# Kernel tuning notes

Hardware: AMD Instinct MI355X
Metric: run time of the kernel (lower is better)

## Reference

```python
import jax, jax.numpy as jnp
import numpy as np

D_STATE = 128   # Mamba2 default (the SS2D d_state=16 is never forwarded to Mamba2)
N_HEADS = 4     # d_ssm // headdim = d_model / (d_model//4)
D_CONV = 4
EPS = 1e-5


def silu(v):
    return v * jax.nn.sigmoid(v)


def setup_inputs() -> dict:
    key = jax.random.key(0)
    ks = jax.random.split(key, 12)
    d_model = 256
    d_inner = 2 * d_model            # expand=2
    d_ssm = d_model
    conv_dim = d_ssm + 2 * D_STATE   # 512
    d_in_proj = 2 * d_inner + 2 * D_STATE + N_HEADS  # 1284
    B, H, W = 8, 64, 64
    inp = {
        "x": jax.random.normal(ks[0], (B, d_model, H, W), jnp.float32),
        "in_proj_w": jax.random.normal(ks[1], (d_in_proj, d_model), jnp.float32) * 0.02,
        "conv_w": jax.random.normal(ks[2], (conv_dim, D_CONV), jnp.float32) * 0.2,
        "conv_b": jnp.zeros((conv_dim,), jnp.float32),
        "dt_bias": jax.random.normal(ks[3], (N_HEADS,), jnp.float32) * 0.1,
        "A_log": jnp.log(jax.random.uniform(ks[4], (N_HEADS,), jnp.float32, 1.0, 16.0)),
        "D": jax.random.normal(ks[5], (N_HEADS,), jnp.float32),
        "norm_w": jnp.ones((d_ssm,), jnp.float32),
        "out_proj_w": jax.random.normal(ks[6], (d_model, d_inner), jnp.float32) * 0.02,
        "se_w1": jax.random.normal(ks[7], (d_model // 4, d_model), jnp.float32) * 0.05,
        "se_b1": jnp.zeros((d_model // 4,), jnp.float32),
        "se_w2": jax.random.normal(ks[8], (d_model, d_model // 4), jnp.float32) * 0.05,
        "se_b2": jnp.zeros((d_model,), jnp.float32),
    }
    return inp


def _forward(x, in_proj_w, conv_w, conv_b, dt_bias, A_log, D, norm_w,
             out_proj_w, se_w1, se_b1, se_w2, se_b2):
    Bb, C, H, W = x.shape
    L = H * W
    d_model = C
    d_inner = 2 * d_model
    d_ssm = d_model
    d_mlp = d_inner - d_ssm
    headdim = d_ssm // N_HEADS
    conv_dim = d_ssm + 2 * D_STATE

    u = x.reshape(Bb, C, L).transpose(0, 2, 1)              # (b, l, c)
    zxbcdt = u @ in_proj_w.T                                 # (b, l, 1284)
    z0 = zxbcdt[..., :d_mlp]
    x0 = zxbcdt[..., d_mlp:2 * d_mlp]
    z = zxbcdt[..., 2 * d_mlp:2 * d_mlp + d_ssm]
    xBC = zxbcdt[..., 2 * d_mlp + d_ssm:2 * d_mlp + d_ssm + conv_dim]
    dt = zxbcdt[..., -N_HEADS:]

    dt = jax.nn.softplus(dt + dt_bias)                       # (b, l, h)

    # causal depthwise conv along l, kernel size D_CONV
    xpad = jnp.pad(xBC, ((0, 0), (D_CONV - 1, 0), (0, 0)))
    xconv = conv_b
    for k in range(D_CONV):
        xconv = xconv + xpad[:, k:k + L, :] * conv_w[:, k]
    xconv = silu(xconv)

    xs = xconv[..., :d_ssm]
    Bm = xconv[..., d_ssm:d_ssm + D_STATE]                   # (b, l, n) ngroups=1
    Cm = xconv[..., d_ssm + D_STATE:]                        # (b, l, n)
    xh = xs.reshape(Bb, L, N_HEADS, headdim)                 # (b, l, h, p)

    A = -jnp.exp(A_log)                                      # (h,)

    def step(hstate, inp):
        xt, dtt, Bt, Ct = inp  # (b,h,p), (b,h), (b,n), (b,n)
        dA = jnp.exp(dtt * A)                                # (b, h)
        hstate = hstate * dA[:, :, None, None] + \
            (dtt[:, :, None, None] * xt[..., None]) * Bt[:, None, None, :]
        y = jnp.einsum('bhpn,bn->bhp', hstate, Ct)
        return hstate, y

    h0 = jnp.zeros((Bb, N_HEADS, headdim, D_STATE), x.dtype)
    _, ys = jax.lax.scan(
        step, h0,
        (xh.transpose(1, 0, 2, 3), dt.transpose(1, 0, 2),
         Bm.transpose(1, 0, 2), Cm.transpose(1, 0, 2)))
    y = ys.transpose(1, 0, 2, 3)                             # (b, l, h, p)
    y = y + D[None, None, :, None] * xh                      # skip
    y = y.reshape(Bb, L, d_ssm)

    # gated RMSNorm (norm_before_gate=False): gate then normalize
    y = y * silu(z)
    y = y * jax.lax.rsqrt(jnp.mean(y * y, axis=-1, keepdims=True) + EPS) * norm_w

    y = jnp.concatenate([silu(z0) * x0, y], axis=-1)         # (b, l, d_inner)
    out = y @ out_proj_w.T                                   # (b, l, d_model)
    out = out.transpose(0, 2, 1).reshape(Bb, C, H, W)

    # SE-style spectral attention
    s = out.mean(axis=(2, 3))                                # (b, c)
    s = jax.nn.relu(s @ se_w1.T + se_b1)
    s = jax.nn.sigmoid(s @ se_w2.T + se_b2)
    return out * s[:, :, None, None]


def reference(x, in_proj_w, conv_w, conv_b, dt_bias, A_log, D, norm_w,
              out_proj_w, se_w1, se_b1, se_w2, se_b2):
    return _forward(x, in_proj_w, conv_w, conv_b, dt_bias, A_log, D, norm_w,
                    out_proj_w, se_w1, se_b1, se_w2, se_b2)
```

## Files before the change

### kernel.cpp

```cpp
#include <hip/hip_runtime.h>
#include <stdint.h>

typedef __attribute__((ext_vector_type(8))) short bf16x8;
typedef __attribute__((ext_vector_type(4))) float f32x4;

__device__ __forceinline__ float bf2f(unsigned short u) {
  unsigned int x = ((unsigned int)u) << 16;
  return __builtin_bit_cast(float, x);
}
__device__ __forceinline__ unsigned short f2bf(float f) {
  unsigned int x = __builtin_bit_cast(unsigned int, f);
  unsigned int r = x + 0x7FFFu + ((x >> 16) & 1u);
  return (unsigned short)(r >> 16);
}
__device__ __forceinline__ float silu(float v) { return v / (1.f + __expf(-v)); }
__device__ __forceinline__ f32x4 fz4() { f32x4 z; z[0]=0.f; z[1]=0.f; z[2]=0.f; z[3]=0.f; return z; }

#define LSEQ 4096
#define DMODEL 256
#define NIN 1284
#define NINP 1408

__global__ __launch_bounds__(256) void k_prep(const float* __restrict__ w_in,
                                              const float* __restrict__ w_out,
                                              unsigned short* __restrict__ wpad,
                                              unsigned short* __restrict__ woutbf,
                                              const float* __restrict__ x,
                                              unsigned short* __restrict__ ubf,
                                              float* __restrict__ smean) {
  int bid = blockIdx.x;
  int tid = threadIdx.x;
  if (bid < 1920) {
    if (bid < 8) smean[bid * 256 + tid] = 0.f;
    int idx = bid * 256 + tid;
    const int tot1 = NINP * DMODEL;
    if (idx < tot1) {
      int n = idx / DMODEL, k = idx % DMODEL;
      int src = (n < 512) ? ((n & 1) ? 256 + (n >> 1) : (n >> 1)) : n;
      float v = (src < NIN) ? w_in[src * DMODEL + k] : 0.f;
      wpad[idx] = f2bf(v);
    } else {
      int j = idx - tot1;
      woutbf[j] = f2bf(w_out[j]);
    }
    return;
  }
  __shared__ float t[64][65];
  int r = (bid - 1920) & 255;
  int b = (bid - 1920) >> 8;
  int lt = r >> 2, kt = r & 3;
  int l0 = lt * 64, k0 = kt * 64;
  int j = tid & 63, i0 = tid >> 6;
  for (int rr = 0; rr < 16; rr++) {
    int ki = i0 + rr * 4;
    t[ki][j] = x[(size_t)(b * DMODEL + k0 + ki) * LSEQ + l0 + j];
  }
  __syncthreads();
  for (int rr = 0; rr < 16; rr++) {
    int li = i0 + rr * 4;
    ubf[(size_t)(b * LSEQ + l0 + li) * DMODEL + k0 + j] = f2bf(t[j][li]);
  }
}

template <int KDIM, int LDA, int LDB, int EPI>
__global__ __launch_bounds__(256) void k_gemm(const unsigned short* __restrict__ A,
                                              const unsigned short* __restrict__ B,
                                              float* __restrict__ outF,
                                              unsigned short* __restrict__ outBF,
                                              unsigned short* __restrict__ outBF2,
                                              float* __restrict__ dtb, int tilesN) {
  __shared__ __align__(16) short lds[17408];
  short* As = lds;
  short* Bs = lds + 8192;
  int nwg = gridDim.x;
  int orig = blockIdx.x;
  int wgid = (nwg & 7) ? orig : ((orig & 7) * (nwg >> 3) + (orig >> 3));
  int tn = wgid % tilesN, tm = wgid / tilesN;
  int m0 = tm * 128, n0 = tn * 128;
  int tid = threadIdx.x;
  int w = tid >> 6, lane = tid & 63;
  int wr = w >> 1, wc = w & 1;
  f32x4 acc[4][4];
  for (int i = 0; i < 4; i++)
    for (int j = 0; j < 4; j++) acc[i][j] = fz4();

  for (int kt = 0; kt < KDIM / 64; kt++) {
    int k0 = kt * 64;
    for (int i = 0; i < 4; i++) {
      int rowblk = w * 32 + i * 8;
      int row = rowblk + (lane >> 3);
      int kc = ((lane & 7) ^ (row & 7)) * 8;
      const unsigned short* ga = A + (size_t)(m0 + row) * LDA + k0 + kc;
      __builtin_amdgcn_global_load_lds((const __attribute__((address_space(1))) unsigned int*)ga,
                                       (__attribute__((address_space(3))) unsigned int*)&As[rowblk * 64],
                                       16, 0, 0);
      const unsigned short* gb = B + (size_t)(n0 + row) * LDB + k0 + kc;
      __builtin_amdgcn_global_load_lds((const __attribute__((address_space(1))) unsigned int*)gb,
                                       (__attribute__((address_space(3))) unsigned int*)&Bs[rowblk * 64],
                                       16, 0, 0);
    }
    __syncthreads();
    for (int kk = 0; kk < 64; kk += 32) {
      int gq = (kk >> 3) + (lane >> 4);
      bf16x8 af[4], bfr[4];
      for (int mi = 0; mi < 4; mi++) {
        int rt = wr * 64 + mi * 16 + (lane & 15);
        af[mi] = *(const bf16x8*)((const char*)As + rt * 128 + ((gq ^ (rt & 7)) << 4));
      }
      for (int ni = 0; ni < 4; ni++) {
        int rs = wc * 64 + ni * 16 + (lane & 15);
        bfr[ni] = *(const bf16x8*)((const char*)Bs + rs * 128 + ((gq ^ (rs & 7)) << 4));
      }
      for (int mi = 0; mi < 4; mi++)
        for (int ni = 0; ni < 4; ni++)
          acc[mi][ni] = __builtin_amdgcn_mfma_f32_16x16x32_bf16(af[mi], bfr[ni], acc[mi][ni], 0, 0, 0);
    }
    __syncthreads();
  }

  int fq = lane >> 4, fr = lane & 15;
  if constexpr (EPI == 1) {
    short* Ctl = lds;
    for (int mi = 0; mi < 4; mi++)
      for (int ni = 0; ni < 4; ni++)
        for (int j = 0; j < 4; j++) {
          int r = wr * 64 + mi * 16 + fq * 4 + j;
          int cch = wc * 64 + ni * 16 + fr;
          Ctl[cch * 136 + r] = (short)f2bf(acc[mi][ni][j]);
        }
    __syncthreads();
    int b = m0 >> 12, l0 = m0 & 4095;
    for (int it = 0; it < 4; it++) {
      int row = it * 32 + (tid >> 3);
      int cc = (tid & 7) * 16;
      uint4 v0 = *(const uint4*)&Ctl[row * 136 + cc];
      uint4 v1 = *(const uint4*)&Ctl[row * 136 + cc + 8];
      unsigned short* dst = outBF + ((size_t)(b * 256 + n0 + row)) * 4096 + l0 + cc;
      *(uint4*)dst = v0;
      *(uint4*)&dst[8] = v1;
    }
    {
      int cch = tid >> 1, hf = tid & 1;
      const short* prow = &Ctl[cch * 136 + hf * 64];
      float s = 0.f;
      for (int q = 0; q < 8; q++) {
        uint4 v = *(const uint4*)&prow[q * 8];
        const unsigned short* pv = (const unsigned short*)&v;
#pragma unroll
        for (int e = 0; e < 8; e++) s += bf2f(pv[e]);
      }
      s += __shfl_xor(s, 1, 64);
      if (!hf) atomicAdd(&dtb[b * 256 + n0 + cch], s);
    }
  } else if constexpr (EPI == 2) {
    unsigned short* xbc = (unsigned short*)outF;
    if (n0 >= 1280) {
      if (wc == 0 && fr < 4) {
        for (int mi = 0; mi < 4; mi++)
          for (int j = 0; j < 4; j++) {
            int m = m0 + wr * 64 + mi * 16 + fq * 4 + j;
            dtb[m * 4 + fr] = acc[mi][0][j];
          }
      }
    } else if (n0 < 512) {
      short* Ct = lds;
      for (int mi = 0; mi < 4; mi++)
        for (int ni = 0; ni < 4; ni++)
          for (int j = 0; j < 4; j++) {
            float v = acc[mi][ni][j];
            float vp = __shfl_xor(v, 1, 64);
            if (!(fr & 1)) {
              float zc = silu(v) * vp;
              Ct[(wr * 64 + mi * 16 + fq * 4 + j) * 72 + wc * 32 + ni * 8 + (fr >> 1)] =
                  (short)f2bf(zc);
            }
          }
      __syncthreads();
      int r = tid >> 1, base = (tid & 1) * 32;
      for (int it = 0; it < 4; it++) {
        int cc = base + it * 8;
        uint4 v = *(const uint4*)&Ct[r * 72 + cc];
        *(uint4*)&outBF[(size_t)(m0 + r) * 512 + (n0 >> 1) + cc] = v;
      }
    } else {
      short* Ct = lds;
      for (int mi = 0; mi < 4; mi++)
        for (int ni = 0; ni < 4; ni++)
          for (int j = 0; j < 4; j++)
            Ct[(wr * 64 + mi * 16 + fq * 4 + j) * 136 + wc * 64 + ni * 16 + fr] =
                (short)f2bf(acc[mi][ni][j]);
      __syncthreads();
      int rr = tid >> 4, cc = (tid & 15) * 8;
      for (int it = 0; it < 8; it++) {
        int r = it * 16 + rr;
        uint4 v = *(const uint4*)&Ct[r * 136 + cc];
        if (n0 < 768) *(uint4*)&outBF2[(size_t)(m0 + r) * 256 + (n0 - 512) + cc] = v;
        else *(uint4*)&xbc[(size_t)(m0 + r) * 512 + (n0 - 768) + cc] = v;
      }
    }
  } else {
    bool dttile = (n0 >= 1280);
    if (dttile) {
      if (wc == 0 && fr < 4) {
        for (int mi = 0; mi < 4; mi++)
          for (int j = 0; j < 4; j++) {
            int m = m0 + wr * 64 + mi * 16 + fq * 4 + j;
            dtb[m * 4 + fr] = acc[mi][0][j];
          }
      }
    } else {
      short* Ct = lds;
      for (int mi = 0; mi < 4; mi++)
        for (int ni = 0; ni < 4; ni++)
          for (int j = 0; j < 4; j++)
            Ct[(wr * 64 + mi * 16 + fq * 4 + j) * 136 + wc * 64 + ni * 16 + fr] =
                (short)f2bf(acc[mi][ni][j]);
      __syncthreads();
      int rr = tid >> 4, cc = (tid & 15) * 8;
      for (int it = 0; it < 8; it++) {
        int r = it * 16 + rr;
        uint4 v = *(const uint4*)&Ct[r * 136 + cc];
        *(uint4*)&outBF[(size_t)(m0 + r) * 1280 + n0 + cc] = v;
      }
    }
  }
}

__global__ __launch_bounds__(256) void k_conv(const unsigned short* __restrict__ src, int stride,
                                              const float* __restrict__ conv_w,
                                              const float* __restrict__ conv_b,
                                              unsigned short* __restrict__ xs,
                                              unsigned short* __restrict__ bc,
                                              unsigned short* __restrict__ xsT,
                                              unsigned short* __restrict__ bT,
                                              const float* __restrict__ dtraw,
                                              const float* __restrict__ dt_bias,
                                              const float* __restrict__ A_log,
                                              float* __restrict__ dts,
                                              float* __restrict__ cums) {
  __shared__ __align__(16) unsigned short xt[35 * 512];
  int bid = blockIdx.x;
  int tid = threadIdx.x;
  if (bid >= 1024) {
    int w4 = tid >> 6, lane = tid & 63;
    int gc = (bid - 1024) * 4 + w4;
    int bh = gc >> 6, cc = gc & 63;
    int b2 = bh >> 2, h2 = bh & 3;
    int t = cc * 64 + lane;
    float v = dtraw[(size_t)(b2 * LSEQ + t) * 4 + h2] + dt_bias[h2];
    float dt = (v > 20.f) ? v : log1pf(__expf(v));
    float Ah = -__expf(A_log[h2]);
    float s = dt * Ah;
    for (int off = 1; off < 64; off <<= 1) {
      float o = __shfl_up(s, off, 64);
      if (lane >= off) s += o;
    }
    dts[bh * LSEQ + t] = dt;
    cums[bh * LSEQ + t] = s;
    return;
  }
  int b = bid >> 7;
  int t0 = (bid & 127) * 32;
  for (int id = tid; id < 35 * 64; id += 256) {
    int r = id >> 6, ch = id & 63;
    int t = t0 - 3 + r;
    float4 v;
    if (t < 0) v = make_float4(0.f, 0.f, 0.f, 0.f);
    else v = *(const float4*)&src[(size_t)(b * LSEQ + t) * stride + ch * 8];
    *(float4*)&xt[r * 512 + ch * 8] = v;
  }
  __syncthreads();
  int c0 = tid, c1 = tid + 256;
  float w0[4], w1[4];
  for (int k = 0; k < 4; k++) { w0[k] = conv_w[c0 * 4 + k]; w1[k] = conv_w[c1 * 4 + k]; }
  float bb0 = conv_b[c0], bb1 = conv_b[c1];
  unsigned short xa0[32], xa1[32];
#pragma unroll
  for (int tl = 0; tl < 32; tl++) {
    float a0 = bb0, a1 = bb1;
    for (int k = 0; k < 4; k++) {
      a0 += bf2f(xt[(tl + k) * 512 + c0]) * w0[k];
      a1 += bf2f(xt[(tl + k) * 512 + c1]) * w1[k];
    }
    a0 = silu(a0); a1 = silu(a1);
    unsigned short u0 = f2bf(a0), u1 = f2bf(a1);
    xa0[tl] = u0; xa1[tl] = u1;
    size_t row = (size_t)(b * LSEQ + t0 + tl);
    xs[row * 256 + c0] = u0;
    bc[row * 256 + (c1 - 256)] = u1;
  }
  if (xsT) {
    const uint4* p0 = (const uint4*)xa0;
    for (int k = 0; k < 4; k++)
      *(uint4*)&xsT[((size_t)(b * 256 + c0)) * LSEQ + t0 + k * 8] = p0[k];
    if (c1 < 384) {
      const uint4* p1 = (const uint4*)xa1;
      for (int k = 0; k < 4; k++)
        *(uint4*)&bT[((size_t)(b * 128 + (c1 - 256))) * LSEQ + t0 + k * 8] = p1[k];
    }
  }
}

__global__ __launch_bounds__(256) void k_scan(const unsigned short* __restrict__ xs,
                                              const unsigned short* __restrict__ bc,
                                              const float* __restrict__ dtb,
                                              const float* __restrict__ dt_bias,
                                              const float* __restrict__ A_log,
                                              const float* __restrict__ Dp,
                                              unsigned short* __restrict__ y) {
  __shared__ __align__(16) unsigned short bcl[32 * 256];
  __shared__ float xsl[32][4];
  __shared__ float dtl[32], dal[32];
  int bid = blockIdx.x;
  int b = bid >> 6;
  int h = (bid >> 4) & 3;
  int pg = bid & 15;
  int tid = threadIdx.x, w = tid >> 6, lane = tid & 63;
  int p = pg * 4 + w;
  float Ah = -expf(A_log[h]);
  float Dh = Dp[h];
  float bias = dt_bias[h];
  float h0 = 0.f, h1 = 0.f;
  for (int t0 = 0; t0 < LSEQ; t0 += 32) {
    for (int id = tid; id < 32 * 32; id += 256) {
      int r = id >> 5, ch = id & 31;
      *(float4*)&bcl[r * 256 + ch * 8] =
          *(const float4*)&bc[(size_t)(b * LSEQ + t0 + r) * 256 + ch * 8];
    }
    if (tid < 128) {
      int r = tid >> 2, pp = tid & 3;
      xsl[r][pp] = bf2f(xs[(size_t)(b * LSEQ + t0 + r) * 256 + h * 64 + pg * 4 + pp]);
    } else if (tid < 160) {
      int r = tid - 128;
      float v = dtb[(size_t)(b * LSEQ + t0 + r) * 4 + h] + bias;
      float dt = (v > 20.f) ? v : log1pf(expf(v));
      dtl[r] = dt;
      dal[r] = expf(dt * Ah);
    }
    __syncthreads();
    for (int tl = 0; tl < 32; tl++) {
      float dtv = dtl[tl], dav = dal[tl], xv = xsl[tl][w];
      float bn  = bf2f(bcl[tl * 256 + lane]);
      float bn2 = bf2f(bcl[tl * 256 + 64 + lane]);
      float cn  = bf2f(bcl[tl * 256 + 128 + lane]);
      float cn2 = bf2f(bcl[tl * 256 + 192 + lane]);
      float coef = dtv * xv;
      h0 = h0 * dav + coef * bn;
      h1 = h1 * dav + coef * bn2;
      float part = h0 * cn + h1 * cn2;
      for (int off = 32; off; off >>= 1) part += __shfl_xor(part, off, 64);
      if (lane == 0)
        y[(size_t)(b * LSEQ + t0 + tl) * 256 + h * 64 + p] = f2bf(part + Dh * xv);
    }
    __syncthreads();
  }
}

__global__ __launch_bounds__(256) void k_chunkA(const unsigned short* __restrict__ bc,
                                                const unsigned short* __restrict__ xsT,
                                                const unsigned short* __restrict__ bT,
                                                const float* __restrict__ dts,
                                                const float* __restrict__ cums,
                                                unsigned short* __restrict__ ST,
                                                unsigned short* __restrict__ yb) {
  __shared__ __align__(16) unsigned short sh[25088];
  unsigned short* Bsm = sh;
  unsigned short* BTs = sh + 8192;
  unsigned short* XT  = sh + 16384;
  unsigned short* Ms  = sh + 20480;
  __shared__ float dtl[64], cuml[64], scl[64];
  int bid = blockIdx.x;
  int bh = bid >> 6, c = bid & 63;
  int b = bh >> 2, h = bh & 3;
  int m0 = b * LSEQ + c * 64;
  int tid = threadIdx.x, w = tid >> 6, lane = tid & 63;

  if (tid < 64) {
    dtl[tid] = dts[bh * LSEQ + c * 64 + tid];
    cuml[tid] = cums[bh * LSEQ + c * 64 + tid];
  }
  __syncthreads();
  float cumQ = cuml[63];

  for (int it = 0; it < 4; it++) {
    int idx = it * 256 + tid, row = idx >> 4, g = idx & 15;
    uint4 v = *(const uint4*)&bc[(size_t)(m0 + row) * 256 + g * 8];
    *(uint4*)((char*)Bsm + row * 256 + ((g ^ (row & 7)) << 4)) = v;
  }
  for (int it = 0; it < 2; it++) {
    int idx = it * 256 + tid, row = idx >> 3, g = idx & 7;
    uint4 v = *(const uint4*)&xsT[((size_t)(b * 256 + h * 64 + row)) * LSEQ + c * 64 + g * 8];
    *(uint4*)((char*)XT + row * 128 + ((g ^ (row & 7)) << 4)) = v;
  }
  if (tid < 64) scl[tid] = dtl[tid] * __expf(cumQ - cuml[tid]);
  __syncthreads();
  for (int it = 0; it < 4; it++) {
    int idx = it * 256 + tid, row = idx >> 3, g = idx & 7;
    uint4 v = *(const uint4*)&bT[((size_t)(b * 128 + row)) * LSEQ + c * 64 + g * 8];
    const unsigned short* pv = (const unsigned short*)&v;
    uint4 o; unsigned short* po = (unsigned short*)&o;
#pragma unroll
    for (int e = 0; e < 8; e++) po[e] = f2bf(bf2f(pv[e]) * scl[g * 8 + e]);
    *(uint4*)((char*)BTs + row * 128 + ((g ^ (row & 7)) << 4)) = o;
  }

  int rt = w * 16 + (lane & 15);
  const unsigned short* arow = bc + (size_t)(m0 + rt) * 256 + 128;
  f32x4 acc1[4];
#pragma unroll
  for (int i = 0; i < 4; i++) acc1[i] = fz4();
#pragma unroll
  for (int ks = 0; ks < 4; ks++) {
    int g = ks * 4 + (lane >> 4);
    bf16x8 a = *(const bf16x8*)&arow[g * 8];
#pragma unroll
    for (int ni = 0; ni < 4; ni++) {
      int rs = ni * 16 + (lane & 15);
      bf16x8 bfr = *(const bf16x8*)((char*)Bsm + rs * 256 + ((g ^ (rs & 7)) << 4));
      acc1[ni] = __builtin_amdgcn_mfma_f32_16x16x32_bf16(a, bfr, acc1[ni], 0, 0, 0);
    }
  }
#pragma unroll
  for (int ni = 0; ni < 4; ni++)
#pragma unroll
    for (int j = 0; j < 4; j++) {
      int t = w * 16 + (lane >> 4) * 4 + j;
      int s = ni * 16 + (lane & 15);
      float v = 0.f;
      if (t >= s) v = acc1[ni][j] * __expf(cuml[t] - cuml[s]) * dtl[s];
      *(unsigned short*)((char*)Ms + t * 128 + (((s >> 3) ^ (t & 7)) << 4) + ((s & 7) << 1)) = f2bf(v);
    }
  __syncthreads();

  f32x4 acc2[4], acc3[8];
#pragma unroll
  for (int i = 0; i < 4; i++) acc2[i] = fz4();
#pragma unroll
  for (int i = 0; i < 8; i++) acc3[i] = fz4();
#pragma unroll
  for (int ks = 0; ks < 2; ks++) {
    int g = ks * 4 + (lane >> 4);
    bf16x8 xf[4];
#pragma unroll
    for (int ni = 0; ni < 4; ni++) {
      int rp = ni * 16 + (lane & 15);
      xf[ni] = *(const bf16x8*)((char*)XT + rp * 128 + ((g ^ (rp & 7)) << 4));
    }
    {
      bf16x8 a = *(const bf16x8*)((char*)Ms + rt * 128 + ((g ^ (rt & 7)) << 4));
#pragma unroll
      for (int ni = 0; ni < 4; ni++)
        acc2[ni] = __builtin_amdgcn_mfma_f32_16x16x32_bf16(a, xf[ni], acc2[ni], 0, 0, 0);
    }
    {
      bf16x8 a3 = xf[w];
#pragma unroll
      for (int ni = 0; ni < 8; ni++) {
        int rn = ni * 16 + (lane & 15);
        bf16x8 bfr = *(const bf16x8*)((char*)BTs + rn * 128 + ((g ^ (rn & 7)) << 4));
        acc3[ni] = __builtin_amdgcn_mfma_f32_16x16x32_bf16(a3, bfr, acc3[ni], 0, 0, 0);
      }
    }
  }
  __syncthreads();
  unsigned short* STst = sh;
#pragma unroll
  for (int ni = 0; ni < 4; ni++)
#pragma unroll
    for (int j = 0; j < 4; j++) {
      int t = w * 16 + (lane >> 4) * 4 + j;
      int p = ni * 16 + (lane & 15);
      Ms[t * 72 + p] = f2bf(acc2[ni][j]);
    }
#pragma unroll
  for (int ni = 0; ni < 8; ni++)
#pragma unroll
    for (int j = 0; j < 4; j++) {
      int p = w * 16 + (lane >> 4) * 4 + j;
      int n = ni * 16 + (lane & 15);
      STst[p * 136 + n] = f2bf(acc3[ni][j]);
    }
  __syncthreads();
  {
    int rr = tid >> 3, cc = (tid & 7) * 8;
    for (int it = 0; it < 2; it++) {
      int t = it * 32 + rr;
      uint4 v = *(const uint4*)&Ms[t * 72 + cc];
      *(uint4*)&yb[(size_t)(m0 + t) * 256 + h * 64 + cc] = v;
    }
  }
  {
    unsigned short* stp = ST + ((size_t)bid << 13);
    int rr = tid >> 2, cc = (tid & 3) * 32;
    for (int q = 0; q < 4; q++) {
      uint4 v = *(const uint4*)&STst[rr * 136 + cc + q * 8];
      *(uint4*)&stp[rr * 128 + cc + q * 8] = v;
    }
  }
}

__global__ __launch_bounds__(256) void k_chunkB(const unsigned short* __restrict__ ST,
                                                const float* __restrict__ cums,
                                                unsigned short* __restrict__ HT) {
  int bid = blockIdx.x;
  int bh = bid >> 3, psl = bid & 7;
  int p = psl * 8 + (threadIdx.x >> 5);
  int n0 = (threadIdx.x & 31) * 4;
  float H[4] = {0.f, 0.f, 0.f, 0.f};
  for (int c = 0; c < 64; c++) {
    size_t base = (size_t)(bh * 64 + c);
    ushort4 hv;
    unsigned short* ha = (unsigned short*)&hv;
#pragma unroll
    for (int e = 0; e < 4; e++) ha[e] = f2bf(H[e]);
    *(ushort4*)&HT[(base * 64 + p) * 128 + n0] = hv;
    ushort4 s4 = *(const ushort4*)&ST[(base << 13) + p * 128 + n0];
    float dec = __expf(cums[bh * LSEQ + c * 64 + 63]);
    H[0] = H[0] * dec + bf2f(s4.x);
    H[1] = H[1] * dec + bf2f(s4.y);
    H[2] = H[2] * dec + bf2f(s4.z);
    H[3] = H[3] * dec + bf2f(s4.w);
  }
}

__global__ __launch_bounds__(256) void k_chunkC2(const unsigned short* __restrict__ bc,
                                                 const unsigned short* __restrict__ xs,
                                                 const unsigned short* __restrict__ zbuf,
                                                 const unsigned short* __restrict__ HT,
                                                 const float* __restrict__ cums,
                                                 const float* __restrict__ Dp,
                                                 const float* __restrict__ norm_w,
                                                 const unsigned short* __restrict__ yb,
                                                 unsigned short* __restrict__ zcat) {
  __shared__ __align__(16) unsigned short Hs[64 * 128];
  __shared__ __align__(16) unsigned short yst[64 * 264];
  __shared__ float nw[256];
  int bid = blockIdx.x;
  int b = bid >> 6, c = bid & 63;
  int m0 = b * LSEQ + c * 64;
  int tid = threadIdx.x, w = tid >> 6, lane = tid & 63;
  if (tid < 256) nw[tid] = norm_w[tid];

  int rt = w * 16 + (lane & 15);
  const unsigned short* arow = bc + (size_t)(m0 + rt) * 256 + 128;
  bf16x8 af[4];
#pragma unroll
  for (int ks = 0; ks < 4; ks++)
    af[ks] = *(const bf16x8*)&arow[(ks * 4 + (lane >> 4)) * 8];

  for (int h = 0; h < 4; h++) {
    int bh = b * 4 + h;
    __syncthreads();
    for (int it = 0; it < 4; it++) {
      int idx = it * 256 + tid, row = idx >> 4, g = idx & 15;
      uint4 v = *(const uint4*)&HT[((size_t)(bh * 64 + c) * 64 + row) * 128 + g * 8];
      *(uint4*)((char*)Hs + row * 256 + ((g ^ (row & 7)) << 4)) = v;
    }
    float exq[4];
    {
      int tb = w * 16 + (lane >> 4) * 4;
#pragma unroll
      for (int j = 0; j < 4; j++) exq[j] = __expf(cums[bh * LSEQ + c * 64 + tb + j]);
    }
    __syncthreads();
    f32x4 acc[4];
#pragma unroll
    for (int i = 0; i < 4; i++) acc[i] = fz4();
#pragma unroll
    for (int ks = 0; ks < 4; ks++) {
      int g = ks * 4 + (lane >> 4);
#pragma unroll
      for (int ni = 0; ni < 4; ni++) {
        int rp = ni * 16 + (lane & 15);
        bf16x8 bfr = *(const bf16x8*)((char*)Hs + rp * 256 + ((g ^ (rp & 7)) << 4));
        acc[ni] = __builtin_amdgcn_mfma_f32_16x16x32_bf16(af[ks], bfr, acc[ni], 0, 0, 0);
      }
    }
#pragma unroll
    for (int ni = 0; ni < 4; ni++)
#pragma unroll
      for (int j = 0; j < 4; j++) {
        int t = w * 16 + (lane >> 4) * 4 + j;
        int p = ni * 16 + (lane & 15);
        yst[t * 264 + h * 64 + p] = f2bf(acc[ni][j] * exq[j]);
      }
  }
  __syncthreads();
  {
    int row = tid >> 2, hh = tid & 3;
    float Dh = Dp[hh];
    size_t moff = (size_t)(m0 + row) * 256 + hh * 64;
    const unsigned short* pyst = &yst[row * 264 + hh * 64];
    float gv[64];
    float ssum = 0.f;
#pragma unroll
    for (int q = 0; q < 8; q++) {
      uint4 vy = *(const uint4*)&yb[moff + q * 8];
      uint4 vx = *(const uint4*)&xs[moff + q * 8];
      uint4 vz = *(const uint4*)&zbuf[moff + q * 8];
      uint4 vi = *(const uint4*)&pyst[q * 8];
      const unsigned short* py = (const unsigned short*)&vy;
      const unsigned short* px = (const unsigned short*)&vx;
      const unsigned short* pz = (const unsigned short*)&vz;
      const unsigned short* pi = (const unsigned short*)&vi;
#pragma unroll
      for (int e = 0; e < 8; e++) {
        float yv = bf2f(py[e]) + bf2f(pi[e]) + Dh * bf2f(px[e]);
        float gg = yv * silu(bf2f(pz[e]));
        gv[q * 8 + e] = gg;
        ssum += gg * gg;
      }
    }
    ssum += __shfl_xor(ssum, 1, 64);
    ssum += __shfl_xor(ssum, 2, 64);
    float inv = rsqrtf(ssum * (1.f / 256.f) + 1e-5f);
#pragma unroll
    for (int q = 0; q < 8; q++) {
      uint4 vo;
      unsigned short* po = (unsigned short*)&vo;
#pragma unroll
      for (int e = 0; e < 8; e++)
        po[e] = f2bf(gv[q * 8 + e] * nw[hh * 64 + q * 8 + e] * inv);
      *(uint4*)&zcat[(size_t)(m0 + row) * 512 + 256 + hh * 64 + q * 8] = vo;
    }
  }
}

template <int MODE>
__global__ __launch_bounds__(256) void k_ycat(const unsigned short* __restrict__ y,
                                              const unsigned short* __restrict__ zsrc,
                                              const float* __restrict__ norm_w,
                                              unsigned short* __restrict__ ocat) {
  int bid = blockIdx.x;
  int tid = threadIdx.x, w = tid >> 6, lane = tid & 63;
  size_t m = (size_t)bid * 4 + w;
  int j0 = lane * 4;
  ushort4 yv = *(const ushort4*)&y[m * 256 + j0];
  ushort4 zv;
  if constexpr (MODE == 0) zv = *(const ushort4*)&zsrc[m * 256 + j0];
  else zv = *(const ushort4*)&zsrc[m * 1280 + 512 + j0];
  unsigned short ya[4] = {yv.x, yv.y, yv.z, yv.w};
  unsigned short za[4] = {zv.x, zv.y, zv.z, zv.w};
  float g[4]; float ssum = 0.f;
  for (int i = 0; i < 4; i++) {
    float gg = bf2f(ya[i]) * silu(bf2f(za[i]));
    g[i] = gg; ssum += gg * gg;
  }
  for (int off = 32; off; off >>= 1) ssum += __shfl_xor(ssum, off, 64);
  float inv = rsqrtf(ssum * (1.f / 256.f) + 1e-5f);
  ushort4 o2;
  unsigned short* o2a = (unsigned short*)&o2;
  for (int i = 0; i < 4; i++) o2a[i] = f2bf(g[i] * norm_w[j0 + i] * inv);
  *(ushort4*)&ocat[m * 512 + 256 + j0] = o2;
  if constexpr (MODE == 1) {
    ushort4 p0 = *(const ushort4*)&zsrc[m * 1280 + 2 * j0];
    ushort4 p1 = *(const ushort4*)&zsrc[m * 1280 + 2 * j0 + 4];
    ushort4 o1;
    unsigned short* o1a = (unsigned short*)&o1;
    o1a[0] = f2bf(silu(bf2f(p0.x)) * bf2f(p0.y));
    o1a[1] = f2bf(silu(bf2f(p0.z)) * bf2f(p0.w));
    o1a[2] = f2bf(silu(bf2f(p1.x)) * bf2f(p1.y));
    o1a[3] = f2bf(silu(bf2f(p1.z)) * bf2f(p1.w));
    *(ushort4*)&ocat[m * 512 + j0] = o1;
  }
}

__global__ __launch_bounds__(512) void k_sefc(const float* __restrict__ smean,
                                              const float* __restrict__ w1, const float* __restrict__ b1,
                                              const float* __restrict__ w2, const float* __restrict__ b2,
                                              float* __restrict__ s2) {
  __shared__ float s1[512];
  int tid = threadIdx.x;
  int b = tid >> 6, j = tid & 63;
  float acc = b1[j];
  for (int k = 0; k < 256; k++) acc += smean[b * 256 + k] * (1.f / 4096.f) * w1[j * 256 + k];
  s1[b * 64 + j] = fmaxf(acc, 0.f);
  __syncthreads();
  for (int idx = tid; idx < 2048; idx += 512) {
    int bb = idx >> 8, c = idx & 255;
    float a2 = b2[c];
    for (int k = 0; k < 64; k++) a2 += s1[bb * 64 + k] * w2[c * 64 + k];
    s2[idx] = 1.f / (1.f + expf(-a2));
  }
}

__global__ __launch_bounds__(256) void k_final(const unsigned short* __restrict__ rest,
                                               const float* __restrict__ s2,
                                               float* __restrict__ out) {
  int row = blockIdx.x;
  float s = s2[row];
  int tid = threadIdx.x;
  const unsigned short* p = rest + (size_t)row * 4096;
  float* o = out + (size_t)row * 4096;
  for (int it = 0; it < 2; it++) {
    int base = (it * 256 + tid) * 8;
    uint4 v = *(const uint4*)&p[base];
    const unsigned short* pv = (const unsigned short*)&v;
    float4 f0, f1;
    f0.x = bf2f(pv[0]) * s; f0.y = bf2f(pv[1]) * s;
    f0.z = bf2f(pv[2]) * s; f0.w = bf2f(pv[3]) * s;
    f1.x = bf2f(pv[4]) * s; f1.y = bf2f(pv[5]) * s;
    f1.z = bf2f(pv[6]) * s; f1.w = bf2f(pv[7]) * s;
    *(float4*)&o[base] = f0;
    *(float4*)&o[base + 4] = f1;
  }
}

extern "C" void kernel_launch(void* const* d_in, const int* in_sizes, int n_in,
                              void* d_out, int out_size, void* d_ws, size_t ws_size,
                              hipStream_t stream) {
  const float* x         = (const float*)d_in[0];
  const float* in_proj_w = (const float*)d_in[1];
  const float* conv_w    = (const float*)d_in[2];
  const float* conv_b    = (const float*)d_in[3];
  const float* dt_bias   = (const float*)d_in[4];
  const float* A_log     = (const float*)d_in[5];
  const float* Dp        = (const float*)d_in[6];
  const float* norm_w    = (const float*)d_in[7];
  const float* out_projw = (const float*)d_in[8];
  const float* se_w1     = (const float*)d_in[9];
  const float* se_b1     = (const float*)d_in[10];
  const float* se_w2     = (const float*)d_in[11];
  const float* se_b2     = (const float*)d_in[12];
  float* out = (float*)d_out;
  char* ws = (char*)d_ws;

  const size_t NEED_CHUNKED = 220676096;

  if (ws_size >= NEED_CHUNKED) {
    unsigned short* ST16  = (unsigned short*)(ws + 0);
    unsigned short* ubf   = (unsigned short*)(ws + 0);
    unsigned short* res16 = (unsigned short*)(ws + 0);
    unsigned short* xbc   = (unsigned short*)(ws + 16777216);
    unsigned short* zcat  = (unsigned short*)(ws + 67108864);
    unsigned short* zbuf  = (unsigned short*)(ws + 100663296);
    unsigned short* xsb   = (unsigned short*)(ws + 117440512);
    unsigned short* bcb   = (unsigned short*)(ws + 134217728);
    unsigned short* HT    = (unsigned short*)(ws + 150994944);
    unsigned short* xsT   = (unsigned short*)(ws + 150994944);
    unsigned short* bT    = (unsigned short*)(ws + 167772160);
    unsigned short* ybuf  = (unsigned short*)(ws + 184549376);
    unsigned short* wpad  = (unsigned short*)(ws + 201326592);
    unsigned short* woutb = (unsigned short*)(ws + 202047488);
    float*          dtraw = (float*)(ws + 202309632);
    float*          dts   = (float*)(ws + 202833920);
    float*          cums  = (float*)(ws + 203358208);
    float*          smean = (float*)(ws + 203882496);
    float*          s2    = (float*)(ws + 203890688);

    k_prep<<<3968, 256, 0, stream>>>(in_proj_w, out_projw, wpad, woutb, x, ubf, smean);
    k_gemm<256, 256, 256, 2><<<256 * 11, 256, 0, stream>>>(ubf, wpad, (float*)xbc, zcat, zbuf, dtraw, 11);
    k_conv<<<1536, 256, 0, stream>>>(xbc, 512, conv_w, conv_b, xsb, bcb, xsT, bT,
                                     dtraw, dt_bias, A_log, dts, cums);
    k_chunkA<<<2048, 256, 0, stream>>>(bcb, xsT, bT, dts, cums, ST16, ybuf);
    k_chunkB<<<256, 256, 0, stream>>>(ST16, cums, HT);
    k_chunkC2<<<512, 256, 0, stream>>>(bcb, xsb, zbuf, HT, cums, Dp, norm_w, ybuf, zcat);
    k_gemm<512, 512, 512, 1><<<256 * 2, 256, 0, stream>>>(zcat, woutb, nullptr, res16, nullptr, smean, 2);
    k_sefc<<<1, 512, 0, stream>>>(smean, se_w1, se_b1, se_w2, se_b2, s2);
    k_final<<<2048, 256, 0, stream>>>(res16, s2, out);
  } else {
    unsigned short* ubf   = (unsigned short*)(ws + 0);
    unsigned short* res16 = (unsigned short*)(ws + 0);
    unsigned short* xsb   = (unsigned short*)(ws + 16777216);
    unsigned short* bcb   = (unsigned short*)(ws + 33554432);
    unsigned short* zx    = (unsigned short*)(ws + 50331648);
    float*          dtb   = (float*)(ws + 134217728);
    unsigned short* ybuf  = (unsigned short*)(ws + 134742016);
    unsigned short* ycat  = (unsigned short*)(ws + 151519232);
    unsigned short* wpad  = (unsigned short*)(ws + 185073664);
    unsigned short* woutb = (unsigned short*)(ws + 185794560);
    float*          smean = (float*)(ws + 186056704);
    float*          s2    = (float*)(ws + 186064896);

    k_prep<<<3968, 256, 0, stream>>>(in_proj_w, out_projw, wpad, woutb, x, ubf, smean);
    k_gemm<256, 256, 256, 0><<<256 * 11, 256, 0, stream>>>(ubf, wpad, nullptr, zx, nullptr, dtb, 11);
    k_conv<<<1024, 256, 0, stream>>>(zx + 768, 1280, conv_w, conv_b, xsb, bcb, nullptr, nullptr,
                                     nullptr, nullptr, nullptr, nullptr, nullptr);
    k_scan<<<512, 256, 0, stream>>>(xsb, bcb, dtb, dt_bias, A_log, Dp, ybuf);
    k_ycat<1><<<8192, 256, 0, stream>>>(ybuf, zx, norm_w, ycat);
    k_gemm<512, 512, 512, 1><<<256 * 2, 256, 0, stream>>>(ycat, woutb, nullptr, res16, nullptr, smean, 2);
    k_sefc<<<1, 512, 0, stream>>>(smean, se_w1, se_b1, se_w2, se_b2, s2);
    k_final<<<2048, 256, 0, stream>>>(res16, s2, out);
  }
}
```

Baseline: 218.2 us.

## Double-buffer GEMM LDS tiles with K-step 32 to overlap loads and MFMA

The bf16 GEMM main loop changes from a single-buffered 64-wide K tile, with two barriers per step, to two LDS buffers of 32-wide K tiles. The next tile is prefetched with global_load_lds while MFMAs run on the current one, leaving one barrier per step. The swizzle changes from XOR on 8 chunks to XOR on 4 chunks to fit the 64-byte rows. The goal is to hide global-load latency. The cost is twice as many loop iterations with less work each, and possibly more LDS bank conflicts from the narrower swizzle.

```diff
diff --git a/kernel.cpp b/kernel.cpp
--- a/kernel.cpp
+++ b/kernel.cpp
@@ -70,8 +70,6 @@
                                               unsigned short* __restrict__ outBF2,
                                               float* __restrict__ dtb, int tilesN) {
   __shared__ __align__(16) short lds[17408];
-  short* As = lds;
-  short* Bs = lds + 8192;
   int nwg = gridDim.x;
   int orig = blockIdx.x;
   int wgid = (nwg & 7) ? orig : ((orig & 7) * (nwg >> 3) + (orig >> 3));
@@ -84,37 +82,49 @@
   for (int i = 0; i < 4; i++)
     for (int j = 0; j < 4; j++) acc[i][j] = fz4();
 
-  for (int kt = 0; kt < KDIM / 64; kt++) {
-    int k0 = kt * 64;
-    for (int i = 0; i < 4; i++) {
-      int rowblk = w * 32 + i * 8;
-      int row = rowblk + (lane >> 3);
-      int kc = ((lane & 7) ^ (row & 7)) * 8;
+  auto stage = [&](int k0, int buf) {
+#pragma unroll
+    for (int i = 0; i < 2; i++) {
+      int rowblk = w * 32 + i * 16;
+      int row = rowblk + (lane >> 2);
+      int kc = (((lane & 3) ^ (row & 3)) << 3);
       const unsigned short* ga = A + (size_t)(m0 + row) * LDA + k0 + kc;
       __builtin_amdgcn_global_load_lds((const __attribute__((address_space(1))) unsigned int*)ga,
-                                       (__attribute__((address_space(3))) unsigned int*)&As[rowblk * 64],
+                                       (__attribute__((address_space(3))) unsigned int*)&lds[buf * 8192 + rowblk * 32],
                                        16, 0, 0);
       const unsigned short* gb = B + (size_t)(n0 + row) * LDB + k0 + kc;
       __builtin_amdgcn_global_load_lds((const __attribute__((address_space(1))) unsigned int*)gb,
-                                       (__attribute__((address_space(3))) unsigned int*)&Bs[rowblk * 64],
+                                       (__attribute__((address_space(3))) unsigned int*)&lds[buf * 8192 + 4096 + rowblk * 32],
                                        16, 0, 0);
     }
-    __syncthreads();
-    for (int kk = 0; kk < 64; kk += 32) {
-      int gq = (kk >> 3) + (lane >> 4);
-      bf16x8 af[4], bfr[4];
-      for (int mi = 0; mi < 4; mi++) {
-        int rt = wr * 64 + mi * 16 + (lane & 15);
-        af[mi] = *(const bf16x8*)((const char*)As + rt * 128 + ((gq ^ (rt & 7)) << 4));
-      }
-      for (int ni = 0; ni < 4; ni++) {
-        int rs = wc * 64 + ni * 16 + (lane & 15);
-        bfr[ni] = *(const bf16x8*)((const char*)Bs + rs * 128 + ((gq ^ (rs & 7)) << 4));
-      }
-      for (int mi = 0; mi < 4; mi++)
-        for (int ni = 0; ni < 4; ni++)
-          acc[mi][ni] = __builtin_amdgcn_mfma_f32_16x16x32_bf16(af[mi], bfr[ni], acc[mi][ni], 0, 0, 0);
-    }
+  };
+
+  stage(0, 0);
+  __syncthreads();
+
+  const int nsteps = KDIM / 32;
+  for (int t = 0; t < nsteps; t++) {
+    int cur = t & 1;
+    if (t + 1 < nsteps) stage((t + 1) * 32, cur ^ 1);
+    int gq = lane >> 4;
+    const char* Abase = (const char*)&lds[cur * 8192];
+    const char* Bbase = (const char*)&lds[cur * 8192 + 4096];
+    bf16x8 af[4], bfr[4];
+#pragma unroll
+    for (int mi = 0; mi < 4; mi++) {
+      int rt = wr * 64 + mi * 16 + (lane & 15);
+      af[mi] = *(const bf16x8*)(Abase + rt * 64 + ((gq ^ (rt & 3)) << 4));
+    }
+#pragma unroll
+    for (int ni = 0; ni < 4; ni++) {
+      int rs = wc * 64 + ni * 16 + (lane & 15);
+      bfr[ni] = *(const bf16x8*)(Bbase + rs * 64 + ((gq ^ (rs & 3)) << 4));
+    }
+#pragma unroll
+    for (int mi = 0; mi < 4; mi++)
+#pragma unroll
+      for (int ni = 0; ni < 4; ni++)
+        acc[mi][ni] = __builtin_amdgcn_mfma_f32_16x16x32_bf16(af[mi], bfr[ni], acc[mi][ni], 0, 0, 0);
     __syncthreads();
   }
 
```

New measurement: 216.2 us (median of 2 runs). Within noise of the previous version (-0.9%).
